# Kernel tuning notes

Hardware: AMD Instinct MI355X
Metric: run time of the kernel (lower is better)

The kernel has to match this reference:

```python
import jax, jax.numpy as jnp
import numpy as np

C = 64        # channel_n
HID = 128     # hidden_size
HEADS = 4
HD = 16       # head_dim = embed_dim // heads, embed_dim overwritten to channel_n
INNER = HEADS * HD  # 64
MLP = 64
H = W = 64    # img_size
B = 8
STEPS = 6
IN_CH = 1     # input_channels
SCALE = HD ** -0.5


def conv3x3_reflect(x, w, b):
    # x: [B,C,H,W], w: [O,I,3,3] -- reflect padding like nn.Conv2d(padding_mode='reflect')
    xp = jnp.pad(x, ((0, 0), (0, 0), (1, 1), (1, 1)), mode='reflect')
    y = jax.lax.conv_general_dilated(xp, w, (1, 1), 'VALID',
                                     dimension_numbers=('NCHW', 'OIHW', 'NCHW'))
    return y + b[None, :, None, None]


def layernorm(x, w, b, axes):
    mu = jnp.mean(x, axis=axes, keepdims=True)
    var = jnp.var(x, axis=axes, keepdims=True)
    return (x - mu) * jax.lax.rsqrt(var + 1e-5) * w + b


def localize(t, h, w):
    # t: [B,heads,n,d] -> [B,heads,n,9,d]; zero-padded 3x3 neighbourhoods
    # (equivalent to grouped conv with 9 unit-impulse filters, padding='same')
    b, nh, n, d = t.shape
    g = t.reshape(b, nh, h, w, d)
    gp = jnp.pad(g, ((0, 0), (0, 0), (1, 1), (1, 1), (0, 0)))
    nb = jnp.stack([gp[:, :, i:i + h, j:j + w, :]
                    for i in range(3) for j in range(3)], axis=4)
    return nb.reshape(b, nh, n, 9, d)


def attn_block(t, ln_w, ln_b, qkv_w, out_w, out_b):
    y = layernorm(t, ln_w, ln_b, -1)
    qkv = y @ qkv_w.T                              # [B,n,3*inner]
    q, k, v = jnp.split(qkv, 3, axis=-1)
    to_heads = lambda z: z.reshape(z.shape[0], z.shape[1], HEADS, HD).transpose(0, 2, 1, 3)
    q, k, v = to_heads(q), to_heads(k), to_heads(v)   # [B,h,n,d]
    kl = localize(k, H, W)                          # [B,h,n,9,d]
    vl = localize(v, H, W)
    dots = jnp.einsum('bhnd,bhnkd->bhnk', q, kl) * SCALE
    a = jax.nn.softmax(dots, axis=-1)               # [B,h,n,9]
    o = jnp.einsum('bhnk,bhnkd->bhnd', a, vl)
    o = o.transpose(0, 2, 1, 3).reshape(t.shape[0], t.shape[1], INNER)
    return o @ out_w.T + out_b


def ff_block(t, ln_w, ln_b, w1, b1, w2, b2):
    y = layernorm(t, ln_w, ln_b, -1)
    y = jax.nn.gelu(y @ w1.T + b1, approximate=False)
    return y @ w2.T + b2


def setup_inputs() -> dict:
    key = jax.random.key(0)
    ks = jax.random.split(key, 20)
    s = 0.02
    inp = {
        'x': jax.random.normal(ks[0], (B, H, W, C), jnp.float32),
        'masks': jax.random.bernoulli(ks[1], 0.5, (STEPS, B, H, W, 1)),
        'p0_w': jax.random.normal(ks[2], (C, C, 3, 3)) * s,
        'p0_b': jnp.zeros((C,)),
        'p1_w': jax.random.normal(ks[3], (C, C, 3, 3)) * s,
        'p1_b': jnp.zeros((C,)),
        'fc0_w': jax.random.normal(ks[4], (HID, 3 * C)) * s,
        'fc0_b': jnp.zeros((HID,)),
        'fc1_w': jax.random.normal(ks[5], (C, HID)) * s,  # zero-init in torch; random here for a non-trivial test
        'norm0_w': jnp.ones((H, W, HID)),
        'norm0_b': jnp.zeros((H, W, HID)),
        'ln1_w': jnp.ones((C,)),
        'ln1_b': jnp.zeros((C,)),
        'qkv_w': jax.random.normal(ks[6], (3 * INNER, C)) * s,
        'out_w': jax.random.normal(ks[7], (C, INNER)) * s,
        'out_b': jnp.zeros((C,)),
        'ln2_w': jnp.ones((C,)),
        'ln2_b': jnp.zeros((C,)),
        'ff1_w': jax.random.normal(ks[8], (MLP, C)) * s,
        'ff1_b': jnp.zeros((MLP,)),
        'ff2_w': jax.random.normal(ks[9], (C, MLP)) * s,
        'ff2_b': jnp.zeros((C,)),
        'steps': STEPS,
    }
    return inp


def reference(x, masks, p0_w, p0_b, p1_w, p1_b, fc0_w, fc0_b, fc1_w,
              norm0_w, norm0_b, ln1_w, ln1_b, qkv_w, out_w, out_b,
              ln2_w, ln2_b, ff1_w, ff1_b, ff2_w, ff2_b, steps):
    def step(xc, mask):
        # ---- NCA perception + update (BackboneNCA.perceive + fc0/relu/norm/fc1) ----
        xt = xc.transpose(0, 3, 1, 2)                      # [B,C,H,W]
        y1 = conv3x3_reflect(xt, p0_w, p0_b)
        y2 = conv3x3_reflect(xt, p1_w, p1_b)
        p = jnp.concatenate([xt, y1, y2], 1).transpose(0, 2, 3, 1)  # [B,H,W,3C]
        hd = jax.nn.relu(p @ fc0_w.T + fc0_b)              # [B,H,W,HID]
        hd = layernorm(hd, norm0_w, norm0_b, (-3, -2, -1))  # norm0 over [H,W,HID]
        dx = hd @ fc1_w.T                                   # [B,H,W,C]
        dx = dx * mask.astype(xc.dtype)                     # stochastic fire
        xn = xc + dx
        # ---- ViT block with localized (3x3 windowed) attention ----
        t = xn.reshape(B, H * W, C)
        t = t + attn_block(t, ln1_w, ln1_b, qkv_w, out_w, out_b)
        t = t + ff_block(t, ln2_w, ln2_b, ff1_w, ff1_b, ff2_w, ff2_b)
        xn = t.reshape(B, H, W, C)
        # keep input channels unchanged
        xn = jnp.concatenate([xc[..., :IN_CH], xn[..., IN_CH:]], axis=-1)
        return xn, None

    out, _ = jax.lax.scan(step, x, masks)
    return out
```

## Files before the change

### kernel.cpp

```cpp
#include <hip/hip_runtime.h>
#include <hip/hip_bf16.h>

typedef __hip_bfloat16 bf16;
typedef __attribute__((ext_vector_type(8))) short bf16x8;
typedef __attribute__((ext_vector_type(4))) float f32x4;

#define NSTEP 6

static __device__ __forceinline__ float b2f(bf16 v) { return __bfloat162float(v); }

static __device__ __forceinline__ float ldp(const void* p, int i, int md) {
    return md ? ((const float*)p)[i] : b2f(((const bf16*)p)[i]);
}
static __device__ __forceinline__ float finz(float v) {
    return (v == v && v * 0.0f == 0.0f) ? v : 0.0f;
}
static __device__ __forceinline__ unsigned short f2bfu(float v) {
    bf16 h = __float2bfloat16(v);
    return *(unsigned short*)&h;
}

static __device__ __forceinline__ void ld_bf8(const bf16* p, float* f) {
    union { uint4 u; unsigned short s[8]; } r;
    r.u = *(const uint4*)p;
#pragma unroll
    for (int j = 0; j < 8; ++j) f[j] = __uint_as_float(((unsigned)r.s[j]) << 16);
}
static __device__ __forceinline__ void ldp8(const void* p, int i, int md, float* f) {
    if (md) {
        const float* fp = (const float*)p + i;
        float4 a = *(const float4*)fp, b = *(const float4*)(fp + 4);
        f[0]=a.x; f[1]=a.y; f[2]=a.z; f[3]=a.w; f[4]=b.x; f[5]=b.y; f[6]=b.z; f[7]=b.w;
    } else {
        ld_bf8((const bf16*)p + i, f);
    }
}
static __device__ __forceinline__ uint4 pk_bf8(const float* f) {
    union { uint4 u; unsigned short s[8]; } r;
#pragma unroll
    for (int j = 0; j < 8; ++j) r.s[j] = f2bfu(f[j]);
    return r.u;
}


__global__ void k_detect(const uint4* __restrict__ m4,
                         const uint4* __restrict__ x4,
                         int* __restrict__ flags, float* __restrict__ accv) {
    __shared__ int s3f, sup, slo, sf32;
    int t = threadIdx.x;
    if (t == 0) { s3f = 0; sup = 0; slo = 0; sf32 = 0; }
    if (t < 96) accv[t] = 0.f;
    __syncthreads();
    int l3f = 0, lup = 0, llo = 0, lf = 0;
    for (int i = t; i < 3072; i += 256) {
        uint4 v = m4[i];
        const unsigned* d = (const unsigned*)&v;
#pragma unroll
        for (int j = 0; j < 4; ++j) {
            unsigned w = d[j];
            unsigned x3f = w ^ 0x3F3F3F3Fu;
            if ((x3f - 0x01010101u) & ~x3f & 0x80808080u) l3f = 1;
            if (w & 0xFFFFFF00u) lup = 1;
            if (w & 0x0000FFFFu) llo = 1;
        }
    }
    for (int i = t; i < 4096; i += 256) {
        uint4 v = x4[i];
        const unsigned* d = (const unsigned*)&v;
#pragma unroll
        for (int j = 0; j < 4; ++j) {
            unsigned bb = (d[j] >> 8) & 0x7Fu;
            if (bb > 0x48u) lf = 1;
        }
    }
    if (l3f) atomicOr(&s3f, 1);
    if (lup) atomicOr(&sup, 1);
    if (llo) atomicOr(&slo, 1);
    if (lf)  atomicOr(&sf32, 1);
    __syncthreads();
    if (t == 0) {
        int mode;
        if (!s3f && !sup) mode = 0;
        else if (!s3f)    mode = 1;
        else if (slo)     mode = 2;
        else              mode = 3;
        flags[0] = mode;
        flags[1] = sf32;
    }
}

__global__ void k_cast(const void* __restrict__ in, float* __restrict__ out,
                       const int* __restrict__ mflags, int n8) {
    int md = mflags[1];
    int i = blockIdx.x * 256 + threadIdx.x;
    if (i < n8) {
        float f[8];
        ldp8(in, i * 8, md, f);
#pragma unroll
        for (int j = 0; j < 8; ++j) f[j] = finz(f[j]);
        *(float4*)&out[i * 8]     = make_float4(f[0], f[1], f[2], f[3]);
        *(float4*)&out[i * 8 + 4] = make_float4(f[4], f[5], f[6], f[7]);
    }
}

__global__ void k_pack_multi(const void* __restrict__ pa, const void* __restrict__ pb,
                             const void* __restrict__ pc, const void* __restrict__ pd,
                             const void* __restrict__ pe, const void* __restrict__ pf,
                             short* __restrict__ out, const int* __restrict__ mflags) {
    int md = mflags[1];
    int i = blockIdx.x * 256 + threadIdx.x;
    if (i >= 57344) return;
    float v;
    if      (i < 24576) v = ldp(pa, i, md);
    else if (i < 32768) v = ldp(pb, i - 24576, md);
    else if (i < 45056) v = ldp(pc, i - 32768, md);
    else if (i < 49152) v = ldp(pd, i - 45056, md);
    else if (i < 53248) v = ldp(pe, i - 49152, md);
    else                v = ldp(pf, i - 53248, md);
    out[i] = (short)f2bfu(v);
}

__global__ void k_pack_bt1(const void* __restrict__ p0, const void* __restrict__ p1,
                           short* __restrict__ out, const int* __restrict__ mflags) {
    int md = mflags[1];
    int i = blockIdx.x * 256 + threadIdx.x;
    if (i < 128 * 576) {
        int o = i / 576, k = i % 576;
        int kk = k >> 6, ii = k & 63;
        float v = (o < 64) ? ldp(p0, o * 576 + ii * 9 + kk, md)
                           : ldp(p1, (o - 64) * 576 + ii * 9 + kk, md);
        out[i] = (short)f2bfu(v);
    }
}

__global__ void k_fold(const void* __restrict__ n0w, const void* __restrict__ n0b,
                       const short* __restrict__ fc1s, float* __restrict__ wsum,
                       float* __restrict__ bconst, const int* __restrict__ mflags) {
    __shared__ short fc1T[128 * 64];
    int md = mflags[1];
    int t = threadIdx.x;
    for (int e = t; e < 8192; e += 256) {
        int c2 = e >> 7, j = e & 127;
        fc1T[j * 64 + c2] = fc1s[c2 * 128 + j];
    }
    __syncthreads();
    int c = t & 63, pl = t >> 6;
    int pos = blockIdx.x * 4 + pl;
    float ws = 0.f, bs = 0.f;
    for (int j = 0; j < 128; ++j) {
        float f = b2f(*(const bf16*)&fc1T[j * 64 + c]);
        ws = fmaf(ldp(n0w, pos * 128 + j, md), f, ws);
        bs = fmaf(ldp(n0b, pos * 128 + j, md), f, bs);
    }
    wsum[pos * 64 + c]   = ws;
    bconst[pos * 64 + c] = bs;
}


__global__ __launch_bounds__(512) void k_perceive(
    const float* __restrict__ xin, const short* __restrict__ bt1,
    const short* __restrict__ fc0s, const short* __restrict__ fc1s,
    const void* __restrict__ p0b, const void* __restrict__ p1b,
    const void* __restrict__ fc0b, const void* __restrict__ n0w,
    const int* __restrict__ mflags, float* __restrict__ t1,
    float* __restrict__ accv, int step)
{
    __shared__ __align__(16) short xpad_s[3 * 66 * 72];
    __shared__ __align__(16) short P_s[64 * 200];
    __shared__ __align__(16) short hd_s[64 * 136];
    __shared__ float red[32];
    int md = mflags[1];
    int bh = blockIdx.x;
    int b = bh >> 6, h = bh & 63;
    int t = threadIdx.x;

    for (int e = t; e < 1536; e += 512) {
        int c8 = e & 7, w = (e >> 3) & 63, r = e >> 9;
        int hr = h - 1 + r; hr = hr < 0 ? -hr : (hr > 63 ? 126 - hr : hr);
        const float* src = xin + ((((b << 6) + hr) << 6) | w) * 64 + c8 * 8;
        float f[8];
        float4 v0 = *(const float4*)src, v1 = *(const float4*)(src + 4);
        f[0]=v0.x; f[1]=v0.y; f[2]=v0.z; f[3]=v0.w; f[4]=v1.x; f[5]=v1.y; f[6]=v1.z; f[7]=v1.w;
        uint4 pv = pk_bf8(f);
        *(uint4*)&xpad_s[((r * 66) + w + 1) * 72 + c8 * 8] = pv;
        if (r == 1) *(uint4*)&P_s[w * 200 + c8 * 8] = pv;
    }
    if (t < 48) {
        int c8 = t & 7, side = (t >> 3) & 1, r = t >> 4;
        int hr = h - 1 + r; hr = hr < 0 ? -hr : (hr > 63 ? 126 - hr : hr);
        int wsrc = side ? 62 : 1, wp = side ? 65 : 0;
        const float* src = xin + ((((b << 6) + hr) << 6) | wsrc) * 64 + c8 * 8;
        float f[8];
        float4 v0 = *(const float4*)src, v1 = *(const float4*)(src + 4);
        f[0]=v0.x; f[1]=v0.y; f[2]=v0.z; f[3]=v0.w; f[4]=v1.x; f[5]=v1.y; f[6]=v1.z; f[7]=v1.w;
        *(uint4*)&xpad_s[((r * 66) + wp) * 72 + c8 * 8] = pk_bf8(f);
    }
    __syncthreads();

    int og  = __builtin_amdgcn_readfirstlane(t >> 6);
    int l   = t & 63, nl = l & 15, q = l >> 4;
    int mt0 = (og & 1) * 2;
    int nt0 = (og >> 1) * 2;
    int o0  = nt0 * 16 + nl, o1 = o0 + 16;

    f32x4 acc[2][2];
#pragma unroll
    for (int i = 0; i < 2; ++i)
#pragma unroll
        for (int j = 0; j < 2; ++j) acc[i][j] = (f32x4){0.f, 0.f, 0.f, 0.f};

    for (int kt = 0; kt < 18; ++kt) {
        int kk = kt >> 1, c0 = (kt & 1) << 5;
        int r = kk / 3, cxi = kk - r * 3;
        bf16x8 b0 = *(const bf16x8*)(bt1 + o0 * 576 + kt * 32 + q * 8);
        bf16x8 b1 = *(const bf16x8*)(bt1 + o1 * 576 + kt * 32 + q * 8);
        bf16x8 a0 = *(const bf16x8*)&xpad_s[((r * 66) + mt0 * 16 + nl + cxi) * 72 + c0 + q * 8];
        bf16x8 a1 = *(const bf16x8*)&xpad_s[((r * 66) + mt0 * 16 + 16 + nl + cxi) * 72 + c0 + q * 8];
        acc[0][0] = __builtin_amdgcn_mfma_f32_16x16x32_bf16(a0, b0, acc[0][0], 0, 0, 0);
        acc[0][1] = __builtin_amdgcn_mfma_f32_16x16x32_bf16(a0, b1, acc[0][1], 0, 0, 0);
        acc[1][0] = __builtin_amdgcn_mfma_f32_16x16x32_bf16(a1, b0, acc[1][0], 0, 0, 0);
        acc[1][1] = __builtin_amdgcn_mfma_f32_16x16x32_bf16(a1, b1, acc[1][1], 0, 0, 0);
    }
    {
        float bias0 = (o0 < 64) ? ldp(p0b, o0, md) : ldp(p1b, o0 - 64, md);
        float bias1 = (o1 < 64) ? ldp(p0b, o1, md) : ldp(p1b, o1 - 64, md);
#pragma unroll
        for (int i = 0; i < 2; ++i)
#pragma unroll
            for (int j = 0; j < 2; ++j) {
                int oo = j ? o1 : o0;
                float bb = j ? bias1 : bias0;
#pragma unroll
                for (int r2 = 0; r2 < 4; ++r2) {
                    int m = (mt0 + i) * 16 + q * 4 + r2;
                    P_s[m * 200 + 64 + oo] = (short)f2bfu(acc[i][j][r2] + bb);
                }
            }
    }
    __syncthreads();

#pragma unroll
    for (int i = 0; i < 2; ++i)
#pragma unroll
        for (int j = 0; j < 2; ++j) acc[i][j] = (f32x4){0.f, 0.f, 0.f, 0.f};
    for (int kt = 0; kt < 6; ++kt) {
        bf16x8 b0 = *(const bf16x8*)(fc0s + o0 * 192 + kt * 32 + q * 8);
        bf16x8 b1 = *(const bf16x8*)(fc0s + o1 * 192 + kt * 32 + q * 8);
        bf16x8 a0 = *(const bf16x8*)&P_s[(mt0 * 16 + nl) * 200 + kt * 32 + q * 8];
        bf16x8 a1 = *(const bf16x8*)&P_s[(mt0 * 16 + 16 + nl) * 200 + kt * 32 + q * 8];
        acc[0][0] = __builtin_amdgcn_mfma_f32_16x16x32_bf16(a0, b0, acc[0][0], 0, 0, 0);
        acc[0][1] = __builtin_amdgcn_mfma_f32_16x16x32_bf16(a0, b1, acc[0][1], 0, 0, 0);
        acc[1][0] = __builtin_amdgcn_mfma_f32_16x16x32_bf16(a1, b0, acc[1][0], 0, 0, 0);
        acc[1][1] = __builtin_amdgcn_mfma_f32_16x16x32_bf16(a1, b1, acc[1][1], 0, 0, 0);
    }
    float lsum = 0.f, lsq = 0.f;
    {
        float fb0 = ldp(fc0b, o0, md), fb1 = ldp(fc0b, o1, md);
#pragma unroll
        for (int i = 0; i < 2; ++i)
#pragma unroll
            for (int j = 0; j < 2; ++j) {
                int oo = j ? o1 : o0;
                float bb = j ? fb1 : fb0;
#pragma unroll
                for (int r2 = 0; r2 < 4; ++r2) {
                    int m = (mt0 + i) * 16 + q * 4 + r2;
                    float v = fmaxf(acc[i][j][r2] + bb, 0.f);
                    unsigned short hu = f2bfu(v);
                    hd_s[m * 136 + oo] = (short)hu;
                    float vr = __uint_as_float(((unsigned)hu) << 16);
                    lsum += vr; lsq += vr * vr;
                }
            }
    }
#pragma unroll
    for (int off = 32; off > 0; off >>= 1) {
        lsum += __shfl_down(lsum, off, 64);
        lsq  += __shfl_down(lsq,  off, 64);
    }
    if (l == 0) { red[og] = lsum; red[16 + og] = lsq; }
    __syncthreads();
    if (t == 0) {
        float a = 0.f, s2 = 0.f;
#pragma unroll
        for (int w = 0; w < 8; ++w) { a += red[w]; s2 += red[16 + w]; }
        atomicAdd(&accv[step * 16 + b * 2],     a);
        atomicAdd(&accv[step * 16 + b * 2 + 1], s2);
    }

    for (int e = t; e < 1024; e += 512) {
        int pos = e >> 4, j8 = (e & 15) * 8;
        float hv[8], wv[8];
        ld_bf8((const bf16*)&hd_s[pos * 136 + j8], hv);
        ldp8(n0w, (h * 64 + pos) * 128 + j8, md, wv);
#pragma unroll
        for (int j = 0; j < 8; ++j) hv[j] *= wv[j];
        *(uint4*)&hd_s[pos * 136 + j8] = pk_bf8(hv);
    }
    __syncthreads();

    {
        int mt = og & 3, nh = og >> 2;
        int to0 = nh * 32 + nl, to1 = to0 + 16;
        f32x4 a0 = (f32x4){0.f,0.f,0.f,0.f}, a1 = (f32x4){0.f,0.f,0.f,0.f};
#pragma unroll
        for (int kt = 0; kt < 4; ++kt) {
            bf16x8 av = *(const bf16x8*)&hd_s[(mt * 16 + nl) * 136 + kt * 32 + q * 8];
            bf16x8 b0 = *(const bf16x8*)(fc1s + to0 * 128 + kt * 32 + q * 8);
            bf16x8 b1 = *(const bf16x8*)(fc1s + to1 * 128 + kt * 32 + q * 8);
            a0 = __builtin_amdgcn_mfma_f32_16x16x32_bf16(av, b0, a0, 0, 0, 0);
            a1 = __builtin_amdgcn_mfma_f32_16x16x32_bf16(av, b1, a1, 0, 0, 0);
        }
#pragma unroll
        for (int r2 = 0; r2 < 4; ++r2) {
            int m = mt * 16 + q * 4 + r2;
            t1[((bh << 6) + m) * 64 + to0] = a0[r2];
            t1[((bh << 6) + m) * 64 + to1] = a1[r2];
        }
    }
}

__global__ __launch_bounds__(512) void k_upd(
    const float* __restrict__ xin, float* __restrict__ xnew,
    const float* __restrict__ t1, const float* __restrict__ wsum,
    const float* __restrict__ bconst, const void* __restrict__ mraw,
    const short* __restrict__ qkvs, const void* __restrict__ ln1w,
    const void* __restrict__ ln1b, const int* __restrict__ mflags,
    const float* __restrict__ accv, bf16* __restrict__ qkv, int step)
{
    __shared__ __align__(16) short ys[64 * 72];
    __shared__ __align__(16) short qo[64 * 200];
    int md = mflags[1];
    int bh = blockIdx.x;
    int b = bh >> 6, h = bh & 63;
    int t = threadIdx.x;
    const float invN = 1.f / 524288.f;
    float mean = accv[step * 16 + b * 2] * invN;
    float var  = accv[step * 16 + b * 2 + 1] * invN - mean * mean;
    float rstd = rsqrtf(fmaxf(var, 0.f) + 1e-5f);
    float mrs  = mean * rstd;

    int tok = t >> 3, j8 = (t & 7) * 8;
    int idx = ((bh << 6) + tok) * 64 + j8;
    int ppos = (h * 64 + tok) * 64 + j8;
    {
        float4 x0 = *(const float4*)&xin[idx], x1 = *(const float4*)&xin[idx + 4];
        float xv[8] = {x0.x, x0.y, x0.z, x0.w, x1.x, x1.y, x1.z, x1.w};
        float4 a0 = *(const float4*)&t1[idx], a1 = *(const float4*)&t1[idx + 4];
        float tv[8] = {a0.x, a0.y, a0.z, a0.w, a1.x, a1.y, a1.z, a1.w};
        float4 w0 = *(const float4*)&wsum[ppos], w1 = *(const float4*)&wsum[ppos + 4];
        float wv[8] = {w0.x, w0.y, w0.z, w0.w, w1.x, w1.y, w1.z, w1.w};
        float4 b0 = *(const float4*)&bconst[ppos], b1 = *(const float4*)&bconst[ppos + 4];
        float bc[8] = {b0.x, b0.y, b0.z, b0.w, b1.x, b1.y, b1.z, b1.w};

        int mmode = mflags[0];
        int midx = ((step * 8 + b) * 64 + h) * 64 + tok;
        int mk;
        if (mmode == 0)      mk = ((const int*)mraw)[midx] != 0;
        else if (mmode == 1) mk = ((const unsigned char*)mraw)[midx] != 0;
        else if (mmode == 2) mk = ((const unsigned short*)mraw)[midx] != 0;
        else                 mk = ((const float*)mraw)[midx] != 0.0f;

        float vloc[8];
        float ls = 0.f, lq = 0.f;
#pragma unroll
        for (int ci = 0; ci < 8; ++ci) {
            float dx = rstd * tv[ci] - mrs * wv[ci] + bc[ci];
            vloc[ci] = finz(mk ? (xv[ci] + dx) : xv[ci]);
            ls += vloc[ci]; lq += vloc[ci] * vloc[ci];
        }
        *(float4*)&xnew[idx]     = make_float4(vloc[0], vloc[1], vloc[2], vloc[3]);
        *(float4*)&xnew[idx + 4] = make_float4(vloc[4], vloc[5], vloc[6], vloc[7]);
#pragma unroll
        for (int off = 1; off < 8; off <<= 1) {
            ls += __shfl_xor(ls, off, 64);
            lq += __shfl_xor(lq, off, 64);
        }
        float mu = ls * (1.f / 64.f);
        float vr = lq * (1.f / 64.f) - mu * mu;
        float rs = rsqrtf(fmaxf(vr, 0.f) + 1e-5f);
        float lw[8], lb[8];
        ldp8(ln1w, j8, md, lw);
        ldp8(ln1b, j8, md, lb);
        float yv[8];
#pragma unroll
        for (int ci = 0; ci < 8; ++ci)
            yv[ci] = (vloc[ci] - mu) * rs * lw[ci] + lb[ci];
        *(uint4*)&ys[tok * 72 + j8] = pk_bf8(yv);
    }
    __syncthreads();

    int og = __builtin_amdgcn_readfirstlane(t >> 6);
    int l = t & 63, nl = l & 15, q = l >> 4;
    {
        int mt = og & 3, nh2 = og >> 2;
        f32x4 qa[6];
#pragma unroll
        for (int n = 0; n < 6; ++n) qa[n] = (f32x4){0.f, 0.f, 0.f, 0.f};
#pragma unroll
        for (int kt = 0; kt < 2; ++kt) {
            bf16x8 av = *(const bf16x8*)&ys[(mt * 16 + nl) * 72 + kt * 32 + q * 8];
#pragma unroll
            for (int n = 0; n < 6; ++n) {
                bf16x8 bv = *(const bf16x8*)(qkvs + (((nh2 * 6 + n) * 16) + nl) * 64 + kt * 32 + q * 8);
                qa[n] = __builtin_amdgcn_mfma_f32_16x16x32_bf16(av, bv, qa[n], 0, 0, 0);
            }
        }
#pragma unroll
        for (int n = 0; n < 6; ++n)
#pragma unroll
            for (int r2 = 0; r2 < 4; ++r2) {
                int m = mt * 16 + q * 4 + r2;
                qo[m * 200 + (nh2 * 6 + n) * 16 + nl] = (short)f2bfu(qa[n][r2]);
            }
    }
    __syncthreads();

    for (int e = t; e < 1536; e += 512) {
        int p2 = e / 24, c8 = e - p2 * 24;
        *(uint4*)(qkv + ((bh << 6) + p2) * 192 + c8 * 8) =
            *(const uint4*)&qo[p2 * 200 + c8 * 8];
    }
}

__global__ __launch_bounds__(512) void k_attn_ff(
    const bf16* __restrict__ qkv, const float* __restrict__ xold,
    float* __restrict__ xnew, const short* __restrict__ outs,
    const short* __restrict__ ff1s, const short* __restrict__ ff2s,
    const void* __restrict__ outb, const void* __restrict__ ln2w,
    const void* __restrict__ ln2b, const void* __restrict__ ff1b,
    const void* __restrict__ ff2b, const int* __restrict__ mflags,
    void* __restrict__ dout, int write_out)
{
    __shared__ __align__(16) char smraw[66240];
    short* Ks = (short*)smraw;
    short* Vs = (short*)(smraw + 28512);
    short* Ao = (short*)(smraw + 57024);
    float* ts = (float*)smraw;
    short* ys = (short*)(smraw + 16640);
    short* hs = (short*)(smraw + 25856);

    int md = mflags[1];
    int bh = blockIdx.x;
    int b = bh >> 6, h = bh & 63;
    int t = threadIdx.x;
    int tok = t >> 3, j8 = (t & 7) * 8;
    int idx = ((bh << 6) + tok) * 64 + j8;

    float xn8[8];
    {
        float4 x0 = *(const float4*)&xnew[idx], x1 = *(const float4*)&xnew[idx + 4];
        xn8[0]=x0.x; xn8[1]=x0.y; xn8[2]=x0.z; xn8[3]=x0.w;
        xn8[4]=x1.x; xn8[5]=x1.y; xn8[6]=x1.z; xn8[7]=x1.w;
    }
    float c0 = (j8 == 0) ? xold[idx] : 0.f;

    if (t < 96) {
        int kind = (t >= 48) ? 1 : 0, u = t - kind * 48;
        int r = u >> 4, side = (u >> 3) & 1, c8 = u & 7;
        short* dst = kind ? Vs : Ks;
        uint4 z = {0, 0, 0, 0};
        *(uint4*)&dst[((r * 66) + (side ? 65 : 0)) * 72 + c8 * 8] = z;
    }
    for (int e = t; e < 3072; e += 512) {
        int kind = (e >= 1536) ? 1 : 0, u = e - kind * 1536;
        int c8 = u & 7, w = (u >> 3) & 63, r = u >> 9;
        int hr = h - 1 + r;
        uint4 v = {0, 0, 0, 0};
        if (hr >= 0 && hr <= 63)
            v = *(const uint4*)(qkv + ((b * 64 + hr) * 64 + w) * 192 + 64 + kind * 64 + c8 * 8);
        short* dst = kind ? Vs : Ks;
        *(uint4*)&dst[((r * 66) + w + 1) * 72 + c8 * 8] = v;
    }
    __syncthreads();

    int head = __builtin_amdgcn_readfirstlane(t >> 6) & 3;
    int pos  = t & 63;
    bool act = t < 256;
    if (act) {
        float qv[16];
        const bf16* qr = qkv + (((b * 64 + h) * 64) + pos) * 192 + head * 16;
        ld_bf8(qr, qv); ld_bf8(qr + 8, qv + 8);

        float a9[9];
#pragma unroll
        for (int r = 0; r < 3; ++r)
#pragma unroll
            for (int cxi = 0; cxi < 3; ++cxi) {
                const short* kp = &Ks[((r * 66) + pos + cxi) * 72 + head * 16];
                float kf[16];
                ld_bf8((const bf16*)kp, kf);
                ld_bf8((const bf16*)(kp + 8), kf + 8);
                float dot = 0.f;
#pragma unroll
                for (int d = 0; d < 16; ++d) dot = fmaf(qv[d], kf[d], dot);
                a9[r * 3 + cxi] = dot * 0.25f;
            }
        float mx = a9[0];
#pragma unroll
        for (int k = 1; k < 9; ++k) mx = fmaxf(mx, a9[k]);
        float ssum = 0.f;
#pragma unroll
        for (int k = 0; k < 9; ++k) { a9[k] = __expf(a9[k] - mx); ssum += a9[k]; }
        float inv = 1.f / ssum;
#pragma unroll
        for (int k = 0; k < 9; ++k) a9[k] *= inv;

        float o[16];
#pragma unroll
        for (int d = 0; d < 16; ++d) o[d] = 0.f;
#pragma unroll
        for (int r = 0; r < 3; ++r)
#pragma unroll
            for (int cxi = 0; cxi < 3; ++cxi) {
                const short* vp = &Vs[((r * 66) + pos + cxi) * 72 + head * 16];
                float vf[16];
                ld_bf8((const bf16*)vp, vf);
                ld_bf8((const bf16*)(vp + 8), vf + 8);
                float w = a9[r * 3 + cxi];
#pragma unroll
                for (int d = 0; d < 16; ++d) o[d] = fmaf(w, vf[d], o[d]);
            }
        *(uint4*)&Ao[pos * 72 + head * 16]     = pk_bf8(o);
        *(uint4*)&Ao[pos * 72 + head * 16 + 8] = pk_bf8(o + 8);
    }
    __syncthreads();

    int og = __builtin_amdgcn_readfirstlane(t >> 6);
    int l = t & 63, nl = l & 15, qd = l >> 4;
    int mt = og & 3;
    int nt0 = (og >> 2) * 2;
    int o0 = nt0 * 16 + nl, o1 = o0 + 16;

    {
        f32x4 pa[2];
        pa[0] = (f32x4){0.f,0.f,0.f,0.f}; pa[1] = (f32x4){0.f,0.f,0.f,0.f};
#pragma unroll
        for (int kt = 0; kt < 2; ++kt) {
            bf16x8 av = *(const bf16x8*)&Ao[(mt * 16 + nl) * 72 + kt * 32 + qd * 8];
            bf16x8 b0 = *(const bf16x8*)(outs + o0 * 64 + kt * 32 + qd * 8);
            bf16x8 b1 = *(const bf16x8*)(outs + o1 * 64 + kt * 32 + qd * 8);
            pa[0] = __builtin_amdgcn_mfma_f32_16x16x32_bf16(av, b0, pa[0], 0, 0, 0);
            pa[1] = __builtin_amdgcn_mfma_f32_16x16x32_bf16(av, b1, pa[1], 0, 0, 0);
        }
        float ob0 = ldp(outb, o0, md), ob1 = ldp(outb, o1, md);
#pragma unroll
        for (int j = 0; j < 2; ++j)
#pragma unroll
            for (int r2 = 0; r2 < 4; ++r2) {
                int m = mt * 16 + qd * 4 + r2;
                ts[m * 65 + (j ? o1 : o0)] = pa[j][r2] + (j ? ob1 : ob0);
            }
    }
    __syncthreads();

    {
        float v[8];
        float ls = 0.f, lq = 0.f;
#pragma unroll
        for (int ci = 0; ci < 8; ++ci) {
            v[ci] = ts[tok * 65 + j8 + ci] + xn8[ci];
            ts[tok * 65 + j8 + ci] = v[ci];
            ls += v[ci]; lq += v[ci] * v[ci];
        }
#pragma unroll
        for (int off = 1; off < 8; off <<= 1) {
            ls += __shfl_xor(ls, off, 64);
            lq += __shfl_xor(lq, off, 64);
        }
        float mu = ls * (1.f / 64.f);
        float vr = lq * (1.f / 64.f) - mu * mu;
        float rs = rsqrtf(fmaxf(vr, 0.f) + 1e-5f);
        float wv[8], bv[8];
        ldp8(ln2w, j8, md, wv);
        ldp8(ln2b, j8, md, bv);
        float yv[8];
#pragma unroll
        for (int ci = 0; ci < 8; ++ci) yv[ci] = (v[ci] - mu) * rs * wv[ci] + bv[ci];
        *(uint4*)&ys[tok * 72 + j8] = pk_bf8(yv);
    }
    __syncthreads();

    {
        f32x4 ma[2];
        ma[0] = (f32x4){0.f,0.f,0.f,0.f}; ma[1] = (f32x4){0.f,0.f,0.f,0.f};
#pragma unroll
        for (int kt = 0; kt < 2; ++kt) {
            bf16x8 av = *(const bf16x8*)&ys[(mt * 16 + nl) * 72 + kt * 32 + qd * 8];
            bf16x8 b0 = *(const bf16x8*)(ff1s + o0 * 64 + kt * 32 + qd * 8);
            bf16x8 b1 = *(const bf16x8*)(ff1s + o1 * 64 + kt * 32 + qd * 8);
            ma[0] = __builtin_amdgcn_mfma_f32_16x16x32_bf16(av, b0, ma[0], 0, 0, 0);
            ma[1] = __builtin_amdgcn_mfma_f32_16x16x32_bf16(av, b1, ma[1], 0, 0, 0);
        }
        float f1b0 = ldp(ff1b, o0, md), f1b1 = ldp(ff1b, o1, md);
#pragma unroll
        for (int j = 0; j < 2; ++j)
#pragma unroll
            for (int r2 = 0; r2 < 4; ++r2) {
                int m = mt * 16 + qd * 4 + r2;
                float v = ma[j][r2] + (j ? f1b1 : f1b0);
                float g = 0.5f * v * (1.f + erff(v * 0.70710678118654752f));
                hs[m * 72 + (j ? o1 : o0)] = (short)f2bfu(g);
            }
    }
    __syncthreads();

    {
        f32x4 fa[2];
        fa[0] = (f32x4){0.f,0.f,0.f,0.f}; fa[1] = (f32x4){0.f,0.f,0.f,0.f};
#pragma unroll
        for (int kt = 0; kt < 2; ++kt) {
            bf16x8 av = *(const bf16x8*)&hs[(mt * 16 + nl) * 72 + kt * 32 + qd * 8];
            bf16x8 b0 = *(const bf16x8*)(ff2s + o0 * 64 + kt * 32 + qd * 8);
            bf16x8 b1 = *(const bf16x8*)(ff2s + o1 * 64 + kt * 32 + qd * 8);
            fa[0] = __builtin_amdgcn_mfma_f32_16x16x32_bf16(av, b0, fa[0], 0, 0, 0);
            fa[1] = __builtin_amdgcn_mfma_f32_16x16x32_bf16(av, b1, fa[1], 0, 0, 0);
        }
        float f2b0 = ldp(ff2b, o0, md), f2b1 = ldp(ff2b, o1, md);
#pragma unroll
        for (int j = 0; j < 2; ++j)
#pragma unroll
            for (int r2 = 0; r2 < 4; ++r2) {
                int m = mt * 16 + qd * 4 + r2;
                int oo = j ? o1 : o0;
                ts[m * 65 + oo] += fa[j][r2] + (j ? f2b1 : f2b0);
            }
    }
    __syncthreads();

    {
        float fv[8];
#pragma unroll
        for (int ci = 0; ci < 8; ++ci) {
            float v = ts[tok * 65 + j8 + ci];
            if (j8 == 0 && ci == 0) v = c0;
            fv[ci] = finz(v);
        }
        *(float4*)&xnew[idx]     = make_float4(fv[0], fv[1], fv[2], fv[3]);
        *(float4*)&xnew[idx + 4] = make_float4(fv[4], fv[5], fv[6], fv[7]);
        if (write_out) {
            if (md) {
                *(float4*)&((float*)dout)[idx]     = make_float4(fv[0], fv[1], fv[2], fv[3]);
                *(float4*)&((float*)dout)[idx + 4] = make_float4(fv[4], fv[5], fv[6], fv[7]);
            } else {
                *(uint4*)&((bf16*)dout)[idx] = pk_bf8(fv);
            }
        }
    }
}


extern "C" void kernel_launch(void* const* d_in, const int* in_sizes, int n_in,
                              void* d_out, int out_size, void* d_ws, size_t ws_size,
                              hipStream_t stream) {
    (void)in_sizes; (void)n_in; (void)out_size; (void)ws_size;
    const void* x     = d_in[0];
    const void* masks = d_in[1];
    const void* p0w   = d_in[2];
    const void* p0b   = d_in[3];
    const void* p1w   = d_in[4];
    const void* p1b   = d_in[5];
    const void* fc0w  = d_in[6];
    const void* fc0b  = d_in[7];
    const void* fc1w  = d_in[8];
    const void* n0w   = d_in[9];
    const void* n0b   = d_in[10];
    const void* ln1w  = d_in[11];
    const void* ln1b  = d_in[12];
    const void* qkvw  = d_in[13];
    const void* outw  = d_in[14];
    const void* outb  = d_in[15];
    const void* ln2w  = d_in[16];
    const void* ln2b  = d_in[17];
    const void* ff1w  = d_in[18];
    const void* ff1b  = d_in[19];
    const void* ff2w  = d_in[20];
    const void* ff2b  = d_in[21];

    char* wsb = (char*)d_ws;
    float* xst0   = (float*)(wsb + 0);
    float* xst1   = (float*)(wsb + 8388608);
    float* t1buf  = (float*)(wsb + 16777216);
    bf16*  qkvb   = (bf16*) (wsb + 25165824);
    short* bt1    = (short*)(wsb + 37748736);
    short* packs  = (short*)(wsb + 37896192);
    float* wsumb  = (float*)(wsb + 38010880);
    float* bconb  = (float*)(wsb + 39059456);
    float* accv   = (float*)(wsb + 40108032);
    int*   mflags = (int*)  (wsb + 40108416);

    short* fc0s = packs;
    short* fc1s = packs + 24576;
    short* qkvs = packs + 32768;
    short* outs = packs + 45056;
    short* ff1s = packs + 49152;
    short* ff2s = packs + 53248;

    k_detect<<<1, 256, 0, stream>>>((const uint4*)masks, (const uint4*)x, mflags, accv);
    k_cast<<<1024, 256, 0, stream>>>(x, xst0, mflags, 262144);
    k_pack_bt1<<<288, 256, 0, stream>>>(p0w, p1w, bt1, mflags);
    k_pack_multi<<<224, 256, 0, stream>>>(fc0w, fc1w, qkvw, outw, ff1w, ff2w, packs, mflags);
    k_fold<<<1024, 256, 0, stream>>>(n0w, n0b, fc1s, wsumb, bconb, mflags);

    float* xbuf[2] = {xst0, xst1};
    for (int s = 0; s < NSTEP; ++s) {
        float* cur = xbuf[s & 1];
        float* nxt = xbuf[(s + 1) & 1];
        k_perceive<<<512, 512, 0, stream>>>(cur, bt1, fc0s, fc1s, p0b, p1b, fc0b,
                                            n0w, mflags, t1buf, accv, s);
        k_upd<<<512, 512, 0, stream>>>(cur, nxt, t1buf, wsumb, bconb, masks,
                                       qkvs, ln1w, ln1b, mflags, accv, qkvb, s);
        k_attn_ff<<<512, 512, 0, stream>>>(qkvb, cur, nxt, outs, ff1s, ff2s,
                                           outb, ln2w, ln2b, ff1b, ff2b, mflags,
                                           d_out, (s == NSTEP - 1) ? 1 : 0);
    }
}
```

Baseline: 577.3 us.

## Fold perception convolutions into fc0 weights and merge prep kernels

Precomputes combined weights by multiplying the two 3x3 perception conv weights (and the identity path) into fc0, so each perceive block runs one 576-deep MFMA GEMM straight from the padded input instead of a conv GEMM followed by a 192-deep fc0 GEMM. This drops the P_s staging buffer, one barrier and the second GEMM loop. The conv biases are folded into a single hidden bias as well. The four setup kernels are merged into one k_prep launch. Rounding now happens once on the combined weights rather than on the intermediate conv outputs, which changes numerics slightly.

```diff
diff --git a/kernel.cpp b/kernel.cpp
--- a/kernel.cpp
+++ b/kernel.cpp
@@ -89,84 +89,86 @@
     }
 }
 
-__global__ void k_cast(const void* __restrict__ in, float* __restrict__ out,
-                       const int* __restrict__ mflags, int n8) {
-    int md = mflags[1];
-    int i = blockIdx.x * 256 + threadIdx.x;
-    if (i < n8) {
-        float f[8];
-        ldp8(in, i * 8, md, f);
-#pragma unroll
-        for (int j = 0; j < 8; ++j) f[j] = finz(f[j]);
-        *(float4*)&out[i * 8]     = make_float4(f[0], f[1], f[2], f[3]);
-        *(float4*)&out[i * 8 + 4] = make_float4(f[4], f[5], f[6], f[7]);
-    }
-}
-
-__global__ void k_pack_multi(const void* __restrict__ pa, const void* __restrict__ pb,
-                             const void* __restrict__ pc, const void* __restrict__ pd,
-                             const void* __restrict__ pe, const void* __restrict__ pf,
-                             short* __restrict__ out, const int* __restrict__ mflags) {
-    int md = mflags[1];
-    int i = blockIdx.x * 256 + threadIdx.x;
-    if (i >= 57344) return;
-    float v;
-    if      (i < 24576) v = ldp(pa, i, md);
-    else if (i < 32768) v = ldp(pb, i - 24576, md);
-    else if (i < 45056) v = ldp(pc, i - 32768, md);
-    else if (i < 49152) v = ldp(pd, i - 45056, md);
-    else if (i < 53248) v = ldp(pe, i - 49152, md);
-    else                v = ldp(pf, i - 53248, md);
-    out[i] = (short)f2bfu(v);
-}
-
-__global__ void k_pack_bt1(const void* __restrict__ p0, const void* __restrict__ p1,
-                           short* __restrict__ out, const int* __restrict__ mflags) {
-    int md = mflags[1];
-    int i = blockIdx.x * 256 + threadIdx.x;
-    if (i < 128 * 576) {
-        int o = i / 576, k = i % 576;
-        int kk = k >> 6, ii = k & 63;
-        float v = (o < 64) ? ldp(p0, o * 576 + ii * 9 + kk, md)
-                           : ldp(p1, (o - 64) * 576 + ii * 9 + kk, md);
-        out[i] = (short)f2bfu(v);
-    }
-}
-
-__global__ void k_fold(const void* __restrict__ n0w, const void* __restrict__ n0b,
-                       const short* __restrict__ fc1s, float* __restrict__ wsum,
-                       float* __restrict__ bconst, const int* __restrict__ mflags) {
+__global__ void k_prep(const void* __restrict__ x, float* __restrict__ xout,
+                       const void* __restrict__ p0w, const void* __restrict__ p1w,
+                       const void* __restrict__ p0b, const void* __restrict__ p1b,
+                       const void* __restrict__ fc0w, const void* __restrict__ fc0b,
+                       const void* __restrict__ fc1w, const void* __restrict__ qkvw,
+                       const void* __restrict__ outw, const void* __restrict__ ff1w,
+                       const void* __restrict__ ff2w,
+                       short* __restrict__ cw, short* __restrict__ packs,
+                       float* __restrict__ hbias,
+                       const void* __restrict__ n0w, const void* __restrict__ n0b,
+                       float* __restrict__ wsum, float* __restrict__ bconst,
+                       const int* __restrict__ mflags) {
     __shared__ short fc1T[128 * 64];
     int md = mflags[1];
     int t = threadIdx.x;
-    for (int e = t; e < 8192; e += 256) {
-        int c2 = e >> 7, j = e & 127;
-        fc1T[j * 64 + c2] = fc1s[c2 * 128 + j];
-    }
-    __syncthreads();
-    int c = t & 63, pl = t >> 6;
-    int pos = blockIdx.x * 4 + pl;
-    float ws = 0.f, bs = 0.f;
-    for (int j = 0; j < 128; ++j) {
-        float f = b2f(*(const bf16*)&fc1T[j * 64 + c]);
-        ws = fmaf(ldp(n0w, pos * 128 + j, md), f, ws);
-        bs = fmaf(ldp(n0b, pos * 128 + j, md), f, bs);
-    }
-    wsum[pos * 64 + c]   = ws;
-    bconst[pos * 64 + c] = bs;
+    int bk = blockIdx.x;
+    if (bk < 1024) {
+        int i = bk * 256 + t;
+        float f[8];
+        ldp8(x, i * 8, md, f);
+#pragma unroll
+        for (int j = 0; j < 8; ++j) f[j] = finz(f[j]);
+        *(float4*)&xout[i * 8]     = make_float4(f[0], f[1], f[2], f[3]);
+        *(float4*)&xout[i * 8 + 4] = make_float4(f[4], f[5], f[6], f[7]);
+    } else if (bk < 1152) {
+        int j = (bk - 1024) * 256 + t;
+        float v;
+        if      (j < 8192)  v = ldp(fc1w, j, md);
+        else if (j < 20480) v = ldp(qkvw, j - 8192, md);
+        else if (j < 24576) v = ldp(outw, j - 20480, md);
+        else if (j < 28672) v = ldp(ff1w, j - 24576, md);
+        else                v = ldp(ff2w, j - 28672, md);
+        packs[j] = (short)f2bfu(v);
+    } else if (bk < 1440) {
+        int p = (bk - 1152) * 4 + (t >> 6);
+        int i = t & 63;
+        int o = p / 9, kk = p - o * 9;
+        float acc = (kk == 4) ? ldp(fc0w, o * 192 + i, md) : 0.f;
+        for (int c = 0; c < 64; ++c) {
+            acc = fmaf(ldp(p0w, c * 576 + i * 9 + kk, md), ldp(fc0w, o * 192 + 64 + c, md), acc);
+            acc = fmaf(ldp(p1w, c * 576 + i * 9 + kk, md), ldp(fc0w, o * 192 + 128 + c, md), acc);
+        }
+        cw[o * 576 + kk * 64 + i] = (short)f2bfu(acc);
+    } else if (bk == 1440) {
+        if (t < 128) {
+            float hb = ldp(fc0b, t, md);
+            for (int c = 0; c < 64; ++c) {
+                hb = fmaf(ldp(p0b, c, md), ldp(fc0w, t * 192 + 64 + c, md), hb);
+                hb = fmaf(ldp(p1b, c, md), ldp(fc0w, t * 192 + 128 + c, md), hb);
+            }
+            hbias[t] = hb;
+        }
+    } else {
+        int fbk = bk - 1441;
+        for (int e = t; e < 8192; e += 256) {
+            int c2 = e >> 7, j = e & 127;
+            fc1T[j * 64 + c2] = (short)f2bfu(ldp(fc1w, c2 * 128 + j, md));
+        }
+        __syncthreads();
+        int c = t & 63, pl = t >> 6;
+        int pos = fbk * 4 + pl;
+        float ws = 0.f, bs = 0.f;
+        for (int j = 0; j < 128; ++j) {
+            float f = b2f(*(const bf16*)&fc1T[j * 64 + c]);
+            ws = fmaf(ldp(n0w, pos * 128 + j, md), f, ws);
+            bs = fmaf(ldp(n0b, pos * 128 + j, md), f, bs);
+        }
+        wsum[pos * 64 + c]   = ws;
+        bconst[pos * 64 + c] = bs;
+    }
 }
 
 
 __global__ __launch_bounds__(512) void k_perceive(
-    const float* __restrict__ xin, const short* __restrict__ bt1,
-    const short* __restrict__ fc0s, const short* __restrict__ fc1s,
-    const void* __restrict__ p0b, const void* __restrict__ p1b,
-    const void* __restrict__ fc0b, const void* __restrict__ n0w,
-    const int* __restrict__ mflags, float* __restrict__ t1,
-    float* __restrict__ accv, int step)
+    const float* __restrict__ xin, const short* __restrict__ cw,
+    const short* __restrict__ fc1s, const float* __restrict__ hbias,
+    const void* __restrict__ n0w, const int* __restrict__ mflags,
+    float* __restrict__ t1, float* __restrict__ accv, int step)
 {
     __shared__ __align__(16) short xpad_s[3 * 66 * 72];
-    __shared__ __align__(16) short P_s[64 * 200];
     __shared__ __align__(16) short hd_s[64 * 136];
     __shared__ float red[32];
     int md = mflags[1];
@@ -181,9 +183,7 @@
         float f[8];
         float4 v0 = *(const float4*)src, v1 = *(const float4*)(src + 4);
         f[0]=v0.x; f[1]=v0.y; f[2]=v0.z; f[3]=v0.w; f[4]=v1.x; f[5]=v1.y; f[6]=v1.z; f[7]=v1.w;
-        uint4 pv = pk_bf8(f);
-        *(uint4*)&xpad_s[((r * 66) + w + 1) * 72 + c8 * 8] = pv;
-        if (r == 1) *(uint4*)&P_s[w * 200 + c8 * 8] = pv;
+        *(uint4*)&xpad_s[((r * 66) + w + 1) * 72 + c8 * 8] = pk_bf8(f);
     }
     if (t < 48) {
         int c8 = t & 7, side = (t >> 3) & 1, r = t >> 4;
@@ -212,8 +212,8 @@
     for (int kt = 0; kt < 18; ++kt) {
         int kk = kt >> 1, c0 = (kt & 1) << 5;
         int r = kk / 3, cxi = kk - r * 3;
-        bf16x8 b0 = *(const bf16x8*)(bt1 + o0 * 576 + kt * 32 + q * 8);
-        bf16x8 b1 = *(const bf16x8*)(bt1 + o1 * 576 + kt * 32 + q * 8);
+        bf16x8 b0 = *(const bf16x8*)(cw + o0 * 576 + kt * 32 + q * 8);
+        bf16x8 b1 = *(const bf16x8*)(cw + o1 * 576 + kt * 32 + q * 8);
         bf16x8 a0 = *(const bf16x8*)&xpad_s[((r * 66) + mt0 * 16 + nl + cxi) * 72 + c0 + q * 8];
         bf16x8 a1 = *(const bf16x8*)&xpad_s[((r * 66) + mt0 * 16 + 16 + nl + cxi) * 72 + c0 + q * 8];
         acc[0][0] = __builtin_amdgcn_mfma_f32_16x16x32_bf16(a0, b0, acc[0][0], 0, 0, 0);
@@ -221,47 +221,16 @@
         acc[1][0] = __builtin_amdgcn_mfma_f32_16x16x32_bf16(a1, b0, acc[1][0], 0, 0, 0);
         acc[1][1] = __builtin_amdgcn_mfma_f32_16x16x32_bf16(a1, b1, acc[1][1], 0, 0, 0);
     }
-    {
-        float bias0 = (o0 < 64) ? ldp(p0b, o0, md) : ldp(p1b, o0 - 64, md);
-        float bias1 = (o1 < 64) ? ldp(p0b, o1, md) : ldp(p1b, o1 - 64, md);
+
+    float lsum = 0.f, lsq = 0.f;
+    {
+        float hb0 = hbias[o0], hb1 = hbias[o1];
 #pragma unroll
         for (int i = 0; i < 2; ++i)
 #pragma unroll
             for (int j = 0; j < 2; ++j) {
                 int oo = j ? o1 : o0;
-                float bb = j ? bias1 : bias0;
-#pragma unroll
-                for (int r2 = 0; r2 < 4; ++r2) {
-                    int m = (mt0 + i) * 16 + q * 4 + r2;
-                    P_s[m * 200 + 64 + oo] = (short)f2bfu(acc[i][j][r2] + bb);
-                }
-            }
-    }
-    __syncthreads();
-
-#pragma unroll
-    for (int i = 0; i < 2; ++i)
-#pragma unroll
-        for (int j = 0; j < 2; ++j) acc[i][j] = (f32x4){0.f, 0.f, 0.f, 0.f};
-    for (int kt = 0; kt < 6; ++kt) {
-        bf16x8 b0 = *(const bf16x8*)(fc0s + o0 * 192 + kt * 32 + q * 8);
-        bf16x8 b1 = *(const bf16x8*)(fc0s + o1 * 192 + kt * 32 + q * 8);
-        bf16x8 a0 = *(const bf16x8*)&P_s[(mt0 * 16 + nl) * 200 + kt * 32 + q * 8];
-        bf16x8 a1 = *(const bf16x8*)&P_s[(mt0 * 16 + 16 + nl) * 200 + kt * 32 + q * 8];
-        acc[0][0] = __builtin_amdgcn_mfma_f32_16x16x32_bf16(a0, b0, acc[0][0], 0, 0, 0);
-        acc[0][1] = __builtin_amdgcn_mfma_f32_16x16x32_bf16(a0, b1, acc[0][1], 0, 0, 0);
-        acc[1][0] = __builtin_amdgcn_mfma_f32_16x16x32_bf16(a1, b0, acc[1][0], 0, 0, 0);
-        acc[1][1] = __builtin_amdgcn_mfma_f32_16x16x32_bf16(a1, b1, acc[1][1], 0, 0, 0);
-    }
-    float lsum = 0.f, lsq = 0.f;
-    {
-        float fb0 = ldp(fc0b, o0, md), fb1 = ldp(fc0b, o1, md);
-#pragma unroll
-        for (int i = 0; i < 2; ++i)
-#pragma unroll
-            for (int j = 0; j < 2; ++j) {
-                int oo = j ? o1 : o0;
-                float bb = j ? fb1 : fb0;
+                float bb = j ? hb1 : hb0;
 #pragma unroll
                 for (int r2 = 0; r2 < 4; ++r2) {
                     int m = (mt0 + i) * 16 + q * 4 + r2;
@@ -682,32 +651,31 @@
     float* xst1   = (float*)(wsb + 8388608);
     float* t1buf  = (float*)(wsb + 16777216);
     bf16*  qkvb   = (bf16*) (wsb + 25165824);
-    short* bt1    = (short*)(wsb + 37748736);
+    short* cw     = (short*)(wsb + 37748736);
     short* packs  = (short*)(wsb + 37896192);
-    float* wsumb  = (float*)(wsb + 38010880);
-    float* bconb  = (float*)(wsb + 39059456);
-    float* accv   = (float*)(wsb + 40108032);
-    int*   mflags = (int*)  (wsb + 40108416);
-
-    short* fc0s = packs;
-    short* fc1s = packs + 24576;
-    short* qkvs = packs + 32768;
-    short* outs = packs + 45056;
-    short* ff1s = packs + 49152;
-    short* ff2s = packs + 53248;
+    float* hbias  = (float*)(wsb + 37961728);
+    float* wsumb  = (float*)(wsb + 37962240);
+    float* bconb  = (float*)(wsb + 39010816);
+    float* accv   = (float*)(wsb + 40059392);
+    int*   mflags = (int*)  (wsb + 40059776);
+
+    short* fc1s = packs;
+    short* qkvs = packs + 8192;
+    short* outs = packs + 20480;
+    short* ff1s = packs + 24576;
+    short* ff2s = packs + 28672;
 
     k_detect<<<1, 256, 0, stream>>>((const uint4*)masks, (const uint4*)x, mflags, accv);
-    k_cast<<<1024, 256, 0, stream>>>(x, xst0, mflags, 262144);
-    k_pack_bt1<<<288, 256, 0, stream>>>(p0w, p1w, bt1, mflags);
-    k_pack_multi<<<224, 256, 0, stream>>>(fc0w, fc1w, qkvw, outw, ff1w, ff2w, packs, mflags);
-    k_fold<<<1024, 256, 0, stream>>>(n0w, n0b, fc1s, wsumb, bconb, mflags);
+    k_prep<<<2465, 256, 0, stream>>>(x, xst0, p0w, p1w, p0b, p1b, fc0w, fc0b,
+                                     fc1w, qkvw, outw, ff1w, ff2w,
+                                     cw, packs, hbias, n0w, n0b, wsumb, bconb, mflags);
 
     float* xbuf[2] = {xst0, xst1};
     for (int s = 0; s < NSTEP; ++s) {
         float* cur = xbuf[s & 1];
         float* nxt = xbuf[(s + 1) & 1];
-        k_perceive<<<512, 512, 0, stream>>>(cur, bt1, fc0s, fc1s, p0b, p1b, fc0b,
-                                            n0w, mflags, t1buf, accv, s);
+        k_perceive<<<512, 512, 0, stream>>>(cur, cw, fc1s, hbias, n0w, mflags,
+                                            t1buf, accv, s);
         k_upd<<<512, 512, 0, stream>>>(cur, nxt, t1buf, wsumb, bconb, masks,
                                        qkvs, ln1w, ln1b, mflags, accv, qkvb, s);
         k_attn_ff<<<512, 512, 0, stream>>>(qkvb, cur, nxt, outs, ff1s, ff2s,
```

Result: no change. 567.2 us (median of 2 runs) (-1.8%).
